# Kernel tuning notes

Hardware: AMD Instinct MI355X
Metric: run time of the kernel (lower is better)

## Reference

```python
import jax, jax.numpy as jnp
import numpy as np

B, T, V, D = 8, 256, 32, 256


def setup_inputs() -> dict:
    key = jax.random.key(0)
    k1, k2 = jax.random.split(key)
    # scale by 0.1 so exp(q.k) stays well within fp32 range (dot std ~ 0.1^2*sqrt(D))
    feature = jax.random.normal(k1, (B, T, V, D), dtype=jnp.float32) * 0.1
    feature_aug = jax.random.normal(k2, (B, T, V, D), dtype=jnp.float32) * 0.1
    return {"feature": feature, "feature_aug": feature_aug}


def reference(feature, feature_aug):
    # match torch permute(0,2,1,3): [B,T,V,D] -> [B,V,T,D]
    f = jnp.transpose(feature, (0, 2, 1, 3))      # [B,V,Tq,D]
    fa = jnp.transpose(feature_aug, (0, 2, 1, 3))  # [B,V,Tk,D]
    # all-pairs QK^T scores: [B_i, B_j, V, Tq, Tk]
    scores = jnp.einsum('ivqd,jvkd->ijvqk', f, fa)
    E = jnp.exp(scores)
    # positive (j == i): ap = exp(scores[i,i]).sum over V, Tq -> [B, Tk]
    diag = jnp.einsum('iivqk->ivqk', E)           # [B,V,Tq,Tk]
    ap_exp = diag.sum(axis=(1, 2))                # [B, Tk]
    # negatives (j != i): sum over j,V,Tk minus the j==i part -> [B, Tq]
    total = E.sum(axis=(1, 2, 4))                 # [B, Tq]
    self_part = diag.sum(axis=(1, 3))             # [B, Tq]
    an_exp = total - self_part                    # [B, Tq]
    # per-anchor loss vector [T]; original sums over anchors then takes .mean()
    loss_vec = -jnp.log(ap_exp / an_exp)          # [B, T]
    return loss_vec.sum(axis=0).mean()
```

## Files before the change

### kernel.cpp

```cpp
#include <hip/hip_runtime.h>
#include <hip/hip_bf16.h>


typedef __attribute__((ext_vector_type(4))) float f32x4;
typedef __attribute__((ext_vector_type(4))) int   i32x4;
typedef __attribute__((ext_vector_type(8))) int   i32x8;
typedef __attribute__((ext_vector_type(8))) __bf16 bf16x8;

#if __has_builtin(__builtin_amdgcn_exp2f)
#define EXP2(x) __builtin_amdgcn_exp2f(x)
#else
#define EXP2(x) exp2f(x)
#endif

#define LOG2E 1.4426950408889634f

#define WAIT_VMCNT(N)                                              \
    do {                                                           \
        asm volatile("s_waitcnt vmcnt(" #N ")" ::: "memory");      \
        __builtin_amdgcn_sched_barrier(0);                         \
    } while (0)
#define WAIT_LGKM0                                                 \
    do {                                                           \
        asm volatile("s_waitcnt lgkmcnt(0)" ::: "memory");         \
        __builtin_amdgcn_sched_barrier(0);                         \
    } while (0)
#define BARRIER()                                                  \
    do {                                                           \
        __builtin_amdgcn_s_barrier();                              \
        __builtin_amdgcn_sched_barrier(0);                         \
    } while (0)

__device__ __forceinline__ unsigned short f2bf(float f) {
    unsigned u = __builtin_bit_cast(unsigned, f);
    u += 0x7FFFu + ((u >> 16) & 1u);
    return (unsigned short)(u >> 16);
}

template <bool HI>
__device__ __forceinline__ unsigned cvt2fp8(float a, float b, unsigned old) {
    return __builtin_amdgcn_cvt_pk_fp8_f32(a, b, old, HI);
}
__device__ __forceinline__ unsigned pack4fp8(float x, float y, float z, float w) {
    return cvt2fp8<true>(z, w, cvt2fp8<false>(x, y, 0u));
}

__device__ __forceinline__ void async16(const void* g, void* l) {
    __builtin_amdgcn_global_load_lds(
        (const __attribute__((address_space(1))) unsigned int*)g,
        (__attribute__((address_space(3))) unsigned int*)l,
        16, 0, 0);
}

__device__ __forceinline__ i32x8 cat8(i32x4 lo, i32x4 hi) {
    i32x8 r;
    r[0] = lo[0]; r[1] = lo[1]; r[2] = lo[2]; r[3] = lo[3];
    r[4] = hi[0]; r[5] = hi[1]; r[6] = hi[2]; r[7] = hi[3];
    return r;
}

template <int CTRL>
__device__ __forceinline__ float dpp_add(float x) {
    int y = __builtin_amdgcn_update_dpp(0, __builtin_bit_cast(int, x),
                                        CTRL, 0xf, 0xf, true);
    return x + __builtin_bit_cast(float, y);
}
__device__ __forceinline__ float rowsum16(float x) {
    x = dpp_add<0x111>(x);
    x = dpp_add<0x112>(x);
    x = dpp_add<0x114>(x);
    x = dpp_add<0x118>(x);
    return x;
}

__global__ __launch_bounds__(256) void infonce_repack_fp8(
    const float* __restrict__ feat_aug, unsigned char* __restrict__ pB,
    float* __restrict__ counters)
{
    const int tid = threadIdx.x;
    if (blockIdx.x == 0) {
        #pragma unroll
        for (int k = 0; k < 24; ++k) counters[k * 256 + tid] = 0.f;
    }
    const unsigned g = blockIdx.x * 256u + (unsigned)tid;
    #pragma unroll
    for (int it = 0; it < 8; ++it) {
        const unsigned idx = it * 524288u + g;
        const float4 f = *(const float4*)(feat_aug + (size_t)idx * 4);
        const unsigned p = pack4fp8(f.x, f.y, f.z, f.w);
        *(unsigned*)(pB + (size_t)idx * 4) = p;
    }
}

__global__ __launch_bounds__(256, 2) void infonce_main_nl(
    const float* __restrict__ feat, const unsigned char* __restrict__ pB,
    float* __restrict__ total, float* __restrict__ selfp, float* __restrict__ ap)
{
    __shared__ __align__(16) unsigned char Stage[32 * 1024];
    __shared__ __align__(16) unsigned char Bs[2][64 * 256];
    float (*ls_row2)[128]  = (float (*)[128])(void*)Stage;
    float (*ls_self2)[128] = (float (*)[128])(void*)(Stage + 1024);

    const int tid  = threadIdx.x;
    const int lane = tid & 63;
    const int w    = tid >> 6;
    const int wm   = w >> 1;
    const int wn   = w & 1;
    const int lrow = lane & 15;
    const int quad = lane >> 4;

    const int tileM = blockIdx.x;
    const int v     = blockIdx.y;
    const int nD0   = (tileM >> 1) * 4;

    const size_t vOff = (size_t)v * 256;

    const size_t rowNbase = (size_t)(w * 16 + quad) * 8192 + vOff;
    #pragma unroll
    for (int nn = 0; nn < 2; ++nn) {
        const unsigned char* srcB = pB + rowNbase + (size_t)nn * 64 * 8192;
        #pragma unroll
        for (int i = 0; i < 4; ++i) {
            const int lg = (lrow ^ ((i * 4 + quad) & 15)) << 4;
            async16(srcB + (size_t)i * 4 * 8192 + lg,
                    &Bs[nn][(w * 16 + i * 4) * 256]);
        }
    }

    i32x8 af[2][4];
    #pragma unroll
    for (int c = 0; c < 4; ++c) {
        #pragma unroll
        for (int i = 0; i < 8; ++i) {
            const int rl = w * 8 + i;
            const int gr = tileM * 128 + c * 32 + rl;
            const int sg = lane ^ (rl & 15);
            async16((const unsigned char*)feat +
                        ((size_t)gr * 8192 + vOff + (size_t)sg * 4) * 4,
                    &Stage[rl * 1024 + lane * 16]);
        }
        WAIT_VMCNT(0);
        BARRIER();
        if ((c >> 1) == wm) {
            #pragma unroll
            for (int tt = 0; tt < 2; ++tt) {
                const int t  = (c & 1) * 2 + tt;
                const int rl = tt * 16 + lrow;
                #pragma unroll
                for (int h = 0; h < 2; ++h) {
                    i32x8 r;
                    #pragma unroll
                    for (int j = 0; j < 8; ++j) {
                        const int G = h * 32 + quad * 8 + j;
                        const float4 f = *(const float4*)
                            &Stage[rl * 1024 + ((G ^ lrow) * 16)];
                        r[j] = pack4fp8(f.x * LOG2E, f.y * LOG2E,
                                        f.z * LOG2E, f.w * LOG2E);
                    }
                    af[h][t] = r;
                }
            }
        }
        WAIT_LGKM0;
        BARRIER();
    }

    float rowp[4][4];
    float selfr[4][4];
    #pragma unroll
    for (int t = 0; t < 4; ++t)
        #pragma unroll
        for (int r = 0; r < 4; ++r) { rowp[t][r] = 0.f; selfr[t][r] = 0.f; }

    auto iterBody = [&](const int n) {
        const int b = n & 1;
        BARRIER();

        i32x8 bfr[2][2];
        #pragma unroll
        for (int h = 0; h < 2; ++h)
            #pragma unroll
            for (int tj = 0; tj < 2; ++tj) {
                const int rB = (wn * 32 + tj * 16 + lrow) * 256;
                const int g0 = ((h * 8 + quad * 2) ^ lrow) * 16;
                bfr[h][tj] = cat8(*(const i32x4*)&Bs[b][rB + g0],
                                  *(const i32x4*)&Bs[b][rB + (g0 ^ 16)]);
            }
        WAIT_LGKM0;
        BARRIER();

        if (n < 30) {
            const unsigned char* src = pB + rowNbase + (size_t)(n + 2) * 64 * 8192;
            #pragma unroll
            for (int i = 0; i < 4; ++i) {
                const int lg = (lrow ^ ((i * 4 + quad) & 15)) << 4;
                async16(src + (size_t)i * 4 * 8192 + lg,
                        &Bs[b][(w * 16 + i * 4) * 256]);
            }
        }

        f32x4 acc[4][2];
        #pragma unroll
        for (int t = 0; t < 4; ++t)
            #pragma unroll
            for (int tj = 0; tj < 2; ++tj)
                acc[t][tj] = (f32x4){0.f, 0.f, 0.f, 0.f};
        __builtin_amdgcn_s_setprio(1);
        #pragma unroll
        for (int h = 0; h < 2; ++h)
            #pragma unroll
            for (int ti = 0; ti < 4; ++ti)
                #pragma unroll
                for (int tj = 0; tj < 2; ++tj)
                    acc[ti][tj] = __builtin_amdgcn_mfma_scale_f32_16x16x128_f8f6f4(
                        af[h][ti], bfr[h][tj], acc[ti][tj],
                        0, 0, 0, 127, 0, 127);
        __builtin_amdgcn_s_setprio(0);

        const bool diagIter = (n >= nD0) && (n < nD0 + 4);
        float colp0 = 0.f, colp1 = 0.f;
        #pragma unroll
        for (int t = 0; t < 4; ++t)
            #pragma unroll
            for (int r = 0; r < 4; ++r) {
                float e0 = EXP2(acc[t][0][r]);
                float e1 = EXP2(acc[t][1][r]);
                rowp[t][r] += e0 + e1;
                if (diagIter) { selfr[t][r] += e0 + e1; colp0 += e0; colp1 += e1; }
            }
        if (diagIter) {
            float q0 = colp0, q1 = colp1;
            q0 += __shfl_xor(q0, 16); q0 += __shfl_xor(q0, 32);
            q1 += __shfl_xor(q1, 16); q1 += __shfl_xor(q1, 32);
            if (lane < 16) {
                atomicAdd(&ap[n * 64 + wn * 32 + lane], q0);
                atomicAdd(&ap[n * 64 + wn * 32 + 16 + lane], q1);
            }
        }
    };

    for (int n = 0; n < 31; ++n) {
        WAIT_VMCNT(4);
        iterBody(n);
    }
    WAIT_VMCNT(0);
    iterBody(31);

    #pragma unroll
    for (int t = 0; t < 4; ++t)
        #pragma unroll
        for (int r = 0; r < 4; ++r) {
            float rs = rowsum16(rowp[t][r]);
            float ss = rowsum16(selfr[t][r]);
            if (lrow == 15) {
                const int idx = wm * 64 + t * 16 + quad * 4 + r;
                ls_row2[wn][idx]  = rs;
                ls_self2[wn][idx] = ss;
            }
        }
    __syncthreads();
    if (tid < 128) {
        atomicAdd(&total[tileM * 128 + tid], ls_row2[0][tid] + ls_row2[1][tid]);
    } else {
        const int t2 = tid - 128;
        atomicAdd(&selfp[tileM * 128 + t2], ls_self2[0][t2] + ls_self2[1][t2]);
    }
}

__global__ __launch_bounds__(256) void infonce_main_slow(
    const float* __restrict__ feat, const float* __restrict__ feat_aug,
    float* __restrict__ total, float* __restrict__ selfp, float* __restrict__ ap)
{
    __shared__ __align__(16) unsigned short As[128][72];
    __shared__ __align__(16) unsigned short Bs[128][72];
    __shared__ float ls_row[128];
    __shared__ float ls_col[128];

    const int tid  = threadIdx.x;
    const int lane = tid & 63;
    const int w    = tid >> 6;
    const int wm   = w >> 1;
    const int wn   = w & 1;
    const int lrow = lane & 15;
    const int quad = lane >> 4;

    const int tileM = blockIdx.x & 15;
    const int tileN = blockIdx.x >> 4;
    const int v     = blockIdx.y;
    const bool diag = (tileM >> 1) == (tileN >> 1);

    if (tid < 128) ls_row[tid] = 0.0f;
    else           ls_col[tid - 128] = 0.0f;

    const float* aBase = feat     + (size_t)v * 256;
    const float* bBase = feat_aug + (size_t)v * 256;

    f32x4 acc[4][4];
    #pragma unroll
    for (int i = 0; i < 4; ++i)
        #pragma unroll
        for (int j = 0; j < 4; ++j)
            acc[i][j] = (f32x4){0.f, 0.f, 0.f, 0.f};

    const int srow = tid >> 4;
    const int scol = (tid & 15) * 4;

    for (int s = 0; s < 4; ++s) {
        const int k0 = s * 64;
        if (s) __syncthreads();
        #pragma unroll
        for (int it = 0; it < 8; ++it) {
            const int row = it * 16 + srow;
            const float4 a4 = *(const float4*)(aBase + (size_t)(tileM * 128 + row) * 8192 + k0 + scol);
            const float4 b4 = *(const float4*)(bBase + (size_t)(tileN * 128 + row) * 8192 + k0 + scol);
            uint2 wa, wb;
            wa.x = (unsigned)f2bf(a4.x) | ((unsigned)f2bf(a4.y) << 16);
            wa.y = (unsigned)f2bf(a4.z) | ((unsigned)f2bf(a4.w) << 16);
            wb.x = (unsigned)f2bf(b4.x) | ((unsigned)f2bf(b4.y) << 16);
            wb.y = (unsigned)f2bf(b4.z) | ((unsigned)f2bf(b4.w) << 16);
            *(uint2*)&As[row][scol] = wa;
            *(uint2*)&Bs[row][scol] = wb;
        }
        __syncthreads();
        #pragma unroll
        for (int kk = 0; kk < 64; kk += 32) {
            bf16x8 af[4], bfr[4];
            #pragma unroll
            for (int t = 0; t < 4; ++t) {
                af[t]  = *(const bf16x8*)&As[wm * 64 + t * 16 + lrow][kk + quad * 8];
                bfr[t] = *(const bf16x8*)&Bs[wn * 64 + t * 16 + lrow][kk + quad * 8];
            }
            #pragma unroll
            for (int ti = 0; ti < 4; ++ti)
                #pragma unroll
                for (int tj = 0; tj < 4; ++tj)
                    acc[ti][tj] = __builtin_amdgcn_mfma_f32_16x16x32_bf16(
                        af[ti], bfr[tj], acc[ti][tj], 0, 0, 0);
        }
    }

    float colp[4] = {0.f, 0.f, 0.f, 0.f};
    #pragma unroll
    for (int ti = 0; ti < 4; ++ti) {
        #pragma unroll
        for (int r = 0; r < 4; ++r) {
            float e0 = __expf(acc[ti][0][r]);
            float e1 = __expf(acc[ti][1][r]);
            float e2 = __expf(acc[ti][2][r]);
            float e3 = __expf(acc[ti][3][r]);
            colp[0] += e0; colp[1] += e1; colp[2] += e2; colp[3] += e3;
            float rp = (e0 + e1) + (e2 + e3);
            rp += __shfl_xor(rp, 1);
            rp += __shfl_xor(rp, 2);
            rp += __shfl_xor(rp, 4);
            rp += __shfl_xor(rp, 8);
            if (lrow == 0)
                atomicAdd(&ls_row[wm * 64 + ti * 16 + quad * 4 + r], rp);
        }
    }
    if (diag) {
        #pragma unroll
        for (int tj = 0; tj < 4; ++tj) {
            float q = colp[tj];
            q += __shfl_xor(q, 16);
            q += __shfl_xor(q, 32);
            if (lane < 16)
                atomicAdd(&ls_col[wn * 64 + tj * 16 + lane], q);
        }
    }
    __syncthreads();
    if (tid < 128) {
        const float rs = ls_row[tid];
        const int rowg = tileM * 128 + tid;
        atomicAdd(&total[rowg], rs);
        if (diag) atomicAdd(&selfp[rowg], rs);
    } else if (diag) {
        const int t2 = tid - 128;
        atomicAdd(&ap[tileN * 128 + t2], ls_col[t2]);
    }
}

__global__ __launch_bounds__(256) void infonce_finalize(
    const float* __restrict__ total, const float* __restrict__ selfp,
    const float* __restrict__ ap, float* __restrict__ out)
{
    __shared__ float red[4];
    const int tid = threadIdx.x;
    float s = 0.f;
    for (int e = tid; e < 2048; e += 256) {
        const float an = total[e] - selfp[e];
        s += logf(an / ap[e]);
    }
    #pragma unroll
    for (int m = 32; m >= 1; m >>= 1) s += __shfl_xor(s, m);
    if ((tid & 63) == 0) red[tid >> 6] = s;
    __syncthreads();
    if (tid == 0) out[0] = (red[0] + red[1] + red[2] + red[3]) * (1.0f / 256.0f);
}

extern "C" void kernel_launch(void* const* d_in, const int* in_sizes, int n_in,
                              void* d_out, int out_size, void* d_ws, size_t ws_size,
                              hipStream_t stream) {
    const float* feat     = (const float*)d_in[0];
    const float* feat_aug = (const float*)d_in[1];
    float* total = (float*)d_ws;
    float* selfp = total + 2048;
    float* ap    = selfp + 2048;

    const size_t packBytes = (size_t)2048 * 8192;
    const size_t need = 32768 + packBytes;
    if (ws_size >= need) {
        unsigned char* pB = (unsigned char*)d_ws + 32768;
        infonce_repack_fp8<<<dim3(2048), 256, 0, stream>>>(feat_aug, pB, total);
        infonce_main_nl<<<dim3(16, 32), 256, 0, stream>>>(feat, pB, total, selfp, ap);
    } else {
        (void)hipMemsetAsync(d_ws, 0, 3 * 2048 * sizeof(float), stream);
        infonce_main_slow<<<dim3(256, 32), 256, 0, stream>>>(feat, feat_aug, total, selfp, ap);
    }
    infonce_finalize<<<1, 256, 0, stream>>>(total, selfp, ap, (float*)d_out);
}
```

Before: 184.7 us.

## Fuse fp8 repack into main kernel with a grid-wide atomic barrier

Drops the separate repack kernel. Each of the 512 main-kernel blocks now converts 4 rows of feature_aug to fp8 while its A-operand staging is done, then all blocks meet at a global atomic-counter barrier before loading B tiles. This removes one kernel launch and lets the repack overlap with A-fragment preparation. The cost is a spin-wait barrier that needs all 512 blocks resident at once (2 per CU at 256 threads) or it deadlocks, plus a small init kernel that resets the counter.

```diff
diff --git a/kernel.cpp b/kernel.cpp
--- a/kernel.cpp
+++ b/kernel.cpp
@@ -73,28 +73,20 @@
     return x;
 }
 
-__global__ __launch_bounds__(256) void infonce_repack_fp8(
-    const float* __restrict__ feat_aug, unsigned char* __restrict__ pB,
-    float* __restrict__ counters)
+__global__ __launch_bounds__(256) void infonce_init(
+    float* __restrict__ counters, unsigned* __restrict__ bar)
 {
     const int tid = threadIdx.x;
-    if (blockIdx.x == 0) {
-        #pragma unroll
-        for (int k = 0; k < 24; ++k) counters[k * 256 + tid] = 0.f;
-    }
-    const unsigned g = blockIdx.x * 256u + (unsigned)tid;
-    #pragma unroll
-    for (int it = 0; it < 8; ++it) {
-        const unsigned idx = it * 524288u + g;
-        const float4 f = *(const float4*)(feat_aug + (size_t)idx * 4);
-        const unsigned p = pack4fp8(f.x, f.y, f.z, f.w);
-        *(unsigned*)(pB + (size_t)idx * 4) = p;
-    }
-}
-
-__global__ __launch_bounds__(256, 2) void infonce_main_nl(
-    const float* __restrict__ feat, const unsigned char* __restrict__ pB,
-    float* __restrict__ total, float* __restrict__ selfp, float* __restrict__ ap)
+    #pragma unroll
+    for (int k = 0; k < 24; ++k) counters[k * 256 + tid] = 0.f;
+    if (tid == 0) *bar = 0u;
+}
+
+__global__ __launch_bounds__(256, 2) void infonce_fused(
+    const float* __restrict__ feat, const float* __restrict__ feat_aug,
+    unsigned char* __restrict__ pB, float* __restrict__ total,
+    float* __restrict__ selfp, float* __restrict__ ap,
+    unsigned* __restrict__ bar)
 {
     __shared__ __align__(16) unsigned char Stage[32 * 1024];
     __shared__ __align__(16) unsigned char Bs[2][64 * 256];
@@ -114,18 +106,6 @@
     const int nD0   = (tileM >> 1) * 4;
 
     const size_t vOff = (size_t)v * 256;
-
-    const size_t rowNbase = (size_t)(w * 16 + quad) * 8192 + vOff;
-    #pragma unroll
-    for (int nn = 0; nn < 2; ++nn) {
-        const unsigned char* srcB = pB + rowNbase + (size_t)nn * 64 * 8192;
-        #pragma unroll
-        for (int i = 0; i < 4; ++i) {
-            const int lg = (lrow ^ ((i * 4 + quad) & 15)) << 4;
-            async16(srcB + (size_t)i * 4 * 8192 + lg,
-                    &Bs[nn][(w * 16 + i * 4) * 256]);
-        }
-    }
 
     i32x8 af[2][4];
     #pragma unroll
@@ -165,6 +145,50 @@
         BARRIER();
     }
 
+    {
+        const int lin = blockIdx.x + 16 * blockIdx.y;
+        #pragma unroll
+        for (int rr = 0; rr < 4; ++rr) {
+            const size_t row = (size_t)(lin * 4 + rr);
+            const float* srcR = feat_aug + row * 8192;
+            unsigned char* dstR = pB + row * 8192;
+            #pragma unroll
+            for (int it = 0; it < 8; ++it) {
+                const int o = (it * 256 + tid) * 4;
+                const float4 f = *(const float4*)(srcR + o);
+                *(unsigned*)(dstR + o) = pack4fp8(f.x, f.y, f.z, f.w);
+            }
+        }
+    }
+
+    WAIT_VMCNT(0);
+    __threadfence();
+    __syncthreads();
+    if (tid == 0) {
+        __hip_atomic_fetch_add(bar, 1u, __ATOMIC_ACQ_REL,
+                               __HIP_MEMORY_SCOPE_AGENT);
+        unsigned got;
+        do {
+            __builtin_amdgcn_s_sleep(4);
+            got = __hip_atomic_load(bar, __ATOMIC_ACQUIRE,
+                                    __HIP_MEMORY_SCOPE_AGENT);
+        } while (got < 512u);
+    }
+    __syncthreads();
+    __threadfence();
+
+    const size_t rowNbase = (size_t)(w * 16 + quad) * 8192 + vOff;
+    #pragma unroll
+    for (int nn = 0; nn < 2; ++nn) {
+        const unsigned char* srcB = pB + rowNbase + (size_t)nn * 64 * 8192;
+        #pragma unroll
+        for (int i = 0; i < 4; ++i) {
+            const int lg = (lrow ^ ((i * 4 + quad) & 15)) << 4;
+            async16(srcB + (size_t)i * 4 * 8192 + lg,
+                    &Bs[nn][(w * 16 + i * 4) * 256]);
+        }
+    }
+
     float rowp[4][4];
     float selfr[4][4];
     #pragma unroll
@@ -406,13 +430,15 @@
     float* total = (float*)d_ws;
     float* selfp = total + 2048;
     float* ap    = selfp + 2048;
+    unsigned* bar = (unsigned*)(ap + 2048);
 
     const size_t packBytes = (size_t)2048 * 8192;
     const size_t need = 32768 + packBytes;
     if (ws_size >= need) {
         unsigned char* pB = (unsigned char*)d_ws + 32768;
-        infonce_repack_fp8<<<dim3(2048), 256, 0, stream>>>(feat_aug, pB, total);
-        infonce_main_nl<<<dim3(16, 32), 256, 0, stream>>>(feat, pB, total, selfp, ap);
+        infonce_init<<<dim3(1), 256, 0, stream>>>(total, bar);
+        infonce_fused<<<dim3(16, 32), 256, 0, stream>>>(
+            feat, feat_aug, pB, total, selfp, ap, bar);
     } else {
         (void)hipMemsetAsync(d_ws, 0, 3 * 2048 * sizeof(float), stream);
         infonce_main_slow<<<dim3(256, 32), 256, 0, stream>>>(feat, feat_aug, total, selfp, ap);
```

Measured after the change: 334.5 us. +81.1%, slower.
